# Performance work log

Hardware: AMD Instinct MI355X
Metric: run time of the kernel (lower is better)

Reference implementation:

```python
import jax, jax.numpy as jnp
import numpy as np

EPS = 1e-5
NEG_SLOPE = 0.2


def batchnorm_nodes(x, gamma, beta):
    # BatchNorm2d over channel=node axis; x: [N, T, D], stats over (T, D) per node
    m = x.mean(axis=(1, 2), keepdims=True)
    v = ((x - m) ** 2).mean(axis=(1, 2), keepdims=True)
    return (x - m) * jax.lax.rsqrt(v + EPS) * gamma[:, None, None] + beta[:, None, None]


def gat_relation(h, src, dst, W, al, ar, N):
    # h: [N, T, D]; W: [D, H, dh]; al/ar: [H, dh]
    z = jnp.einsum('ntd,dhe->nthe', h, W)              # [N, T, H, dh]
    el = jnp.einsum('nthe,he->nth', z, al)             # [N, T, H]
    er = jnp.einsum('nthe,he->nth', z, ar)
    e = jax.nn.leaky_relu(el[src] + er[dst], NEG_SLOPE)  # [E, T, H]
    emax = jax.ops.segment_max(e, dst, num_segments=N)   # [N, T, H]
    ex = jnp.exp(e - emax[dst])
    denom = jax.ops.segment_sum(ex, dst, num_segments=N)
    alpha = ex / jnp.maximum(denom[dst], 1e-16)          # segment softmax over in-edges
    msg = alpha[..., None] * z[src]                      # [E, T, H, dh]
    return jax.ops.segment_sum(msg, dst, num_segments=N)  # [N, T, H, dh]


def setup_inputs() -> dict:
    key = jax.random.key(0)
    ks = jax.random.split(key, 12)
    N, T, D, H, E, DFF = 10000, 12, 64, 4, 100000, 128
    dh = D // H
    s = 0.1
    return {
        'x': jax.random.normal(ks[0], (N, T, D), jnp.float32),
        'src1': jax.random.randint(ks[1], (E,), 0, N, jnp.int32),
        'dst1': jax.random.randint(ks[2], (E,), 0, N, jnp.int32),
        'src2': jax.random.randint(ks[3], (E,), 0, N, jnp.int32),
        'dst2': jax.random.randint(ks[4], (E,), 0, N, jnp.int32),
        'W1': jax.random.normal(ks[5], (D, H, dh), jnp.float32) * s,
        'al1': jax.random.normal(ks[6], (H, dh), jnp.float32) * s,
        'ar1': jax.random.normal(ks[7], (H, dh), jnp.float32) * s,
        'W2': jax.random.normal(ks[8], (D, H, dh), jnp.float32) * s,
        'al2': jax.random.normal(ks[9], (H, dh), jnp.float32) * s,
        'ar2': jax.random.normal(ks[10], (H, dh), jnp.float32) * s,
        'bn1_g': jnp.ones((N,), jnp.float32),
        'bn1_b': jnp.zeros((N,), jnp.float32),
        'bn2_g': jnp.ones((N,), jnp.float32),
        'bn2_b': jnp.zeros((N,), jnp.float32),
        'ff_w1': jax.random.normal(ks[11], (D, DFF), jnp.float32) * s,
        'ff_b1': jnp.zeros((DFF,), jnp.float32),
        'ff_w2': jax.random.normal(jax.random.fold_in(key, 99), (DFF, D), jnp.float32) * s,
        'ff_b2': jnp.zeros((D,), jnp.float32),
    }


def reference(x, src1, dst1, src2, dst2, W1, al1, ar1, W2, al2, ar2,
              bn1_g, bn1_b, bn2_g, bn2_b, ff_w1, ff_b1, ff_w2, ff_b2):
    N, T, D = x.shape
    h = batchnorm_nodes(x, bn1_g, bn1_b)
    # HeteroGraphConv: per-relation GAT, sum aggregation
    m = gat_relation(h, src1, dst1, W1, al1, ar1, N) \
      + gat_relation(h, src2, dst2, W2, al2, ar2, N)   # [N, T, H, dh]
    m = m.reshape(N, T, D)
    x2 = x + m                                          # residual (dropout=identity in eval)
    h2 = batchnorm_nodes(x2, bn2_g, bn2_b)
    ff = jax.nn.gelu(h2 @ ff_w1 + ff_b1, approximate=False) @ ff_w2 + ff_b2
    return x2 + ff
```

## Files before the change

### kernel.cpp

```cpp
#include <hip/hip_runtime.h>
#include <math.h>

constexpr int kT = 12;
constexpr float kNeg = 0.2f;
constexpr float kEps = 1e-5f;
constexpr float kLog2e = 1.44269504088896f;

typedef __attribute__((ext_vector_type(8))) short bf16x8;
typedef __attribute__((ext_vector_type(4))) float f32x4;

__device__ __forceinline__ short f2bf(float f) {
  union { float f; unsigned u; } v;
  v.f = f;
  return (short)((v.u + 0x7fffu + ((v.u >> 16) & 1u)) >> 16);
}
__device__ __forceinline__ unsigned pack2(float a, float b) {
  return (unsigned)(unsigned short)f2bf(a) | ((unsigned)(unsigned short)f2bf(b) << 16);
}

__device__ __forceinline__ float wave_reduce_sum(float v) {
#pragma unroll
  for (int o = 32; o > 0; o >>= 1) v += __shfl_xor(v, o);
  return v;
}

__global__ void prep_kernel(const float* __restrict__ x, const float* __restrict__ g,
                            const float* __restrict__ b, float* __restrict__ scale,
                            float* __restrict__ shift, const float* __restrict__ fw1,
                            const float* __restrict__ fw2, const float* __restrict__ zW1,
                            const float* __restrict__ zW2, const float* __restrict__ al1,
                            const float* __restrict__ ar1, const float* __restrict__ al2,
                            const float* __restrict__ ar2, bf16x8* __restrict__ fw1f,
                            bf16x8* __restrict__ fw2f, bf16x8* __restrict__ zw1f,
                            bf16x8* __restrict__ zw2f, bf16x8* __restrict__ walf,
                            const int* __restrict__ dst1, const int* __restrict__ dst2,
                            int* __restrict__ deg1, int* __restrict__ deg2, int N, int E1,
                            int E2, int nBnBlk) {
  int blk = blockIdx.x;
  int lane = threadIdx.x & 63, wid = threadIdx.x >> 6;
  if (blk < nBnBlk) {
    int n = blk * 4 + wid;
    if (n < N) {
      const float* xr = x + (size_t)n * 768;
      float s = 0.f, s2 = 0.f;
#pragma unroll
      for (int c = 0; c < 3; c++) {
        float4 v = *(const float4*)&xr[c * 256 + lane * 4];
        s += v.x + v.y + v.z + v.w;
        s2 += v.x * v.x + v.y * v.y + v.z * v.z + v.w * v.w;
      }
      s = wave_reduce_sum(s);
      s2 = wave_reduce_sum(s2);
      if (lane == 0) {
        const float inv = 1.f / 768.f;
        float mean = s * inv;
        float var = s2 * inv - mean * mean;
        float sc = rsqrtf(var + kEps) * g[n];
        scale[n] = sc;
        shift[n] = b[n] - mean * sc;
      }
    }
    return;
  }
  blk -= nBnBlk;
  int m = lane & 15, q = lane >> 4;
  if (blk == 0) {
    for (int fi = wid; fi < 16; fi += 4) {
      int mt = fi >> 1, kc = fi & 1;
      bf16x8 v;
#pragma unroll
      for (int j = 0; j < 8; j++) v[j] = f2bf(fw1[(kc * 32 + q * 8 + j) * 128 + mt * 16 + m]);
      fw1f[fi * 64 + lane] = v;
    }
    return;
  }
  if (blk == 1) {
    for (int fi = wid; fi < 16; fi += 4) {
      int mt2 = fi >> 2, kc2 = fi & 3;
      bf16x8 u;
#pragma unroll
      for (int j = 0; j < 8; j++) u[j] = f2bf(fw2[(kc2 * 32 + q * 8 + j) * 64 + mt2 * 16 + m]);
      fw2f[fi * 64 + lane] = u;
    }
    return;
  }
  if (blk == 2) {
    for (int fi = wid; fi < 8; fi += 4) {
      int mt = fi >> 1, kc = fi & 1;
      bf16x8 v, u;
#pragma unroll
      for (int j = 0; j < 8; j++) {
        int d = kc * 32 + q * 8 + j;
        v[j] = f2bf(zW1[d * 64 + mt * 16 + m]);
        u[j] = f2bf(zW2[d * 64 + mt * 16 + m]);
      }
      zw1f[fi * 64 + lane] = v;
      zw2f[fi * 64 + lane] = u;
    }
    return;
  }
  if (blk == 3) {
    __shared__ float wal[16][64];
    for (int e0 = threadIdx.x; e0 < 1024; e0 += 256) {
      int f = e0 >> 6, d = e0 & 63;
      int h = f & 3;
      const float* av = (f < 4) ? al1 : (f < 8) ? ar1 : (f < 12) ? al2 : ar2;
      const float* W = (f < 8) ? zW1 : zW2;
      float s = 0.f;
#pragma unroll
      for (int e = 0; e < 16; e++) s += W[d * 64 + h * 16 + e] * av[h * 16 + e];
      wal[f][d] = s * kLog2e;
    }
    __syncthreads();
    if (wid == 0) {
#pragma unroll
      for (int kc = 0; kc < 2; kc++) {
        bf16x8 v;
#pragma unroll
        for (int j = 0; j < 8; j++) v[j] = f2bf(wal[m][kc * 32 + q * 8 + j]);
        walf[kc * 64 + lane] = v;
      }
    }
    return;
  }
  int i = (blk - 4) * 256 + threadIdx.x;
  if (i < E1) atomicAdd(&deg1[dst1[i]], 1);
  else if (i < E1 + E2) atomicAdd(&deg2[dst2[i - E1]], 1);
}

__global__ void scan_kernel(const int* __restrict__ deg1, int* __restrict__ off1,
                            const int* __restrict__ deg2, int* __restrict__ off2, int N) {
  const int* deg = blockIdx.x ? deg2 : deg1;
  int* off = blockIdx.x ? off2 : off1;
  __shared__ int wsum[16];
  __shared__ int carry;
  int tid = threadIdx.x, lane = tid & 63, wv = tid >> 6;
  if (tid == 0) { carry = 0; off[0] = 0; }
  __syncthreads();
  for (int base = 0; base < N; base += 1024) {
    int i = base + tid;
    int incl = (i < N) ? deg[i] : 0;
#pragma unroll
    for (int o = 1; o < 64; o <<= 1) {
      int y = __shfl_up(incl, o);
      if (lane >= o) incl += y;
    }
    if (lane == 63) wsum[wv] = incl;
    __syncthreads();
    if (tid < 16) {
      int p = wsum[tid];
#pragma unroll
      for (int o = 1; o < 16; o <<= 1) {
        int y = __shfl_up(p, o);
        if (tid >= o) p += y;
      }
      wsum[tid] = p;
    }
    __syncthreads();
    int prefix = carry + (wv > 0 ? wsum[wv - 1] : 0);
    if (i < N) off[i + 1] = prefix + incl;
    int total = carry + wsum[15];
    __syncthreads();
    if (tid == 0) carry = total;
    __syncthreads();
  }
}

__global__ __launch_bounds__(256) void fillzel_kernel(
    const int* __restrict__ src1, const int* __restrict__ dst1, const int* __restrict__ off1,
    int* __restrict__ cur1, int* __restrict__ scsr1, const int* __restrict__ src2,
    const int* __restrict__ dst2, const int* __restrict__ off2, int* __restrict__ cur2,
    int* __restrict__ scsr2, int E1, int E2, int nZelBlk,
    const float* __restrict__ x, const float* __restrict__ scale,
    const float* __restrict__ shift, const bf16x8* __restrict__ zw1f,
    const bf16x8* __restrict__ zw2f, const bf16x8* __restrict__ walf,
    unsigned short* __restrict__ z1, unsigned short* __restrict__ z2,
    float* __restrict__ el1, float* __restrict__ er1, float* __restrict__ el2,
    float* __restrict__ er2, int NT) {
  if ((int)blockIdx.x >= nZelBlk) {
    int i = ((int)blockIdx.x - nZelBlk) * 256 + threadIdx.x;
    if (i < E1) {
      int d = dst1[i];
      int p = atomicAdd(&cur1[d], 1);
      scsr1[off1[d] + p] = src1[i] * kT;
    } else if (i < E1 + E2) {
      int k = i - E1;
      int d = dst2[k];
      int p = atomicAdd(&cur2[d], 1);
      scsr2[off2[d] + p] = src2[k] * kT;
    }
    return;
  }
  __shared__ bf16x8 sW1[8][64];
  __shared__ bf16x8 sW2[8][64];
  __shared__ bf16x8 sWE[2][64];
  int lane = threadIdx.x & 63, wid = threadIdx.x >> 6;
  int m = lane & 15, q = lane >> 4;
  for (int fi = wid; fi < 8; fi += 4) {
    sW1[fi][lane] = zw1f[fi * 64 + lane];
    sW2[fi][lane] = zw2f[fi * 64 + lane];
  }
  if (wid == 0) {
    sWE[0][lane] = walf[lane];
    sWE[1][lane] = walf[64 + lane];
  }
  __syncthreads();
  int ntile = (NT + 15) / 16;
  for (int tile = blockIdx.x * 4 + wid; tile < ntile; tile += nZelBlk * 4) {
    int r0 = tile * 16;
    int row = r0 + m;
    int rowc = (row < NT) ? row : NT - 1;
    int n = rowc / kT;
    float sc = scale[n], sh = shift[n];
    bf16x8 hf[2];
#pragma unroll
    for (int kc = 0; kc < 2; kc++) {
      float4 p0 = *(const float4*)&x[(size_t)rowc * 64 + kc * 32 + q * 8];
      float4 p1 = *(const float4*)&x[(size_t)rowc * 64 + kc * 32 + q * 8 + 4];
      hf[kc][0] = f2bf(fmaf(p0.x, sc, sh));
      hf[kc][1] = f2bf(fmaf(p0.y, sc, sh));
      hf[kc][2] = f2bf(fmaf(p0.z, sc, sh));
      hf[kc][3] = f2bf(fmaf(p0.w, sc, sh));
      hf[kc][4] = f2bf(fmaf(p1.x, sc, sh));
      hf[kc][5] = f2bf(fmaf(p1.y, sc, sh));
      hf[kc][6] = f2bf(fmaf(p1.z, sc, sh));
      hf[kc][7] = f2bf(fmaf(p1.w, sc, sh));
    }
    f32x4 a1[4], a2[4], ae;
#pragma unroll
    for (int mt = 0; mt < 4; mt++) {
      a1[mt] = (f32x4){0.f, 0.f, 0.f, 0.f};
      a2[mt] = (f32x4){0.f, 0.f, 0.f, 0.f};
    }
    ae = (f32x4){0.f, 0.f, 0.f, 0.f};
#pragma unroll
    for (int kc = 0; kc < 2; kc++) {
#pragma unroll
      for (int mt = 0; mt < 4; mt++) {
        a1[mt] = __builtin_amdgcn_mfma_f32_16x16x32_bf16(sW1[mt * 2 + kc][lane], hf[kc],
                                                         a1[mt], 0, 0, 0);
        a2[mt] = __builtin_amdgcn_mfma_f32_16x16x32_bf16(sW2[mt * 2 + kc][lane], hf[kc],
                                                         a2[mt], 0, 0, 0);
      }
      ae = __builtin_amdgcn_mfma_f32_16x16x32_bf16(sWE[kc][lane], hf[kc], ae, 0, 0, 0);
    }
    if (row < NT) {
      float* edst = (q == 0) ? el1 : (q == 1) ? er1 : (q == 2) ? el2 : er2;
      *(float4*)&edst[(size_t)row * 4] = make_float4(ae[0], ae[1], ae[2], ae[3]);
#pragma unroll
      for (int mt = 0; mt < 4; mt++) {
        uint2 u1 = {pack2(a1[mt][0], a1[mt][1]), pack2(a1[mt][2], a1[mt][3])};
        uint2 u2 = {pack2(a2[mt][0], a2[mt][1]), pack2(a2[mt][2], a2[mt][3])};
        *(uint2*)&z1[(size_t)row * 64 + mt * 16 + 4 * q] = u1;
        *(uint2*)&z2[(size_t)row * 64 + mt * 16 + 4 * q] = u2;
      }
    }
  }
}

__device__ __forceinline__ void gat_rel(int n, int t, const int* __restrict__ scsr,
                                        const int* __restrict__ off,
                                        const float* __restrict__ elp, float er_h,
                                        const unsigned short* __restrict__ zp, int lane,
                                        float& a0, float& a1, float& a2, float& a3) {
  int b0 = off[n], b1 = off[n + 1];
  if (b1 <= b0) return;
  float den = 0.f, n0 = 0.f, n1 = 0.f, n2 = 0.f, n3 = 0.f;
  for (int c0 = b0; c0 < b1; c0 += 64) {
    int cnt = b1 - c0;
    if (cnt > 64) cnt = 64;
    int idx = c0 + lane;
    int sbl = scsr[(idx < b1) ? idx : b1 - 1];
    int s0 = __shfl(sbl, 0) + t;
    int s1 = (cnt > 1) ? (__shfl(sbl, 1) + t) : s0;
    int s2 = (cnt > 2) ? (__shfl(sbl, 2) + t) : s1;
    float e0 = elp[(size_t)s0 * 4];
    uint2 z0 = *(const uint2*)(zp + (size_t)s0 * 64);
    float e1 = elp[(size_t)s1 * 4];
    uint2 zz1 = *(const uint2*)(zp + (size_t)s1 * 64);
    float e2 = elp[(size_t)s2 * 4];
    uint2 zz2 = *(const uint2*)(zp + (size_t)s2 * 64);
    for (int k = 0; k < cnt; k++) {
      int s3 = (k + 3 < cnt) ? (__shfl(sbl, k + 3) + t) : s2;
      float e3 = elp[(size_t)s3 * 4];
      uint2 zz3 = *(const uint2*)(zp + (size_t)s3 * 64);
      float ev = e0 + er_h;
      ev = fmaxf(ev, kNeg * ev);
      float wgt = exp2f(ev);
      den += wgt;
      n0 = fmaf(wgt, __uint_as_float(z0.x << 16), n0);
      n1 = fmaf(wgt, __uint_as_float(z0.x & 0xffff0000u), n1);
      n2 = fmaf(wgt, __uint_as_float(z0.y << 16), n2);
      n3 = fmaf(wgt, __uint_as_float(z0.y & 0xffff0000u), n3);
      s0 = s1; e0 = e1; z0 = zz1;
      s1 = s2; e1 = e2; zz1 = zz2;
      s2 = s3; e2 = e3; zz2 = zz3;
    }
  }
  float inv = 1.f / den;
  a0 = fmaf(n0, inv, a0);
  a1 = fmaf(n1, inv, a1);
  a2 = fmaf(n2, inv, a2);
  a3 = fmaf(n3, inv, a3);
}

__global__ __launch_bounds__(256) void agg_kernel(
    const float* __restrict__ x, const int* __restrict__ scsr1,
    const int* __restrict__ off1, const float* __restrict__ el1,
    const float* __restrict__ er1, const unsigned short* __restrict__ z1,
    const int* __restrict__ scsr2, const int* __restrict__ off2,
    const float* __restrict__ el2, const float* __restrict__ er2,
    const unsigned short* __restrict__ z2, float* __restrict__ x2,
    float* __restrict__ bn2s, float* __restrict__ bn2q, int N) {
  int wid = threadIdx.x >> 6, lane = threadIdx.x & 63;
  int w = blockIdx.x * 4 + wid;
  if (w >= N * 3) return;
  int n = w / 3;
  int t0 = (w - n * 3) * 4;
  int tl = lane >> 4, cg = lane & 15;
  int t = t0 + tl;
  int row = n * kT + t;
  int h = cg >> 2;
  float a0 = 0.f, a1 = 0.f, a2 = 0.f, a3 = 0.f;
  gat_rel(n, t, scsr1, off1, el1 + h, er1[(size_t)row * 4 + h], z1 + cg * 4, lane, a0, a1, a2,
          a3);
  gat_rel(n, t, scsr2, off2, el2 + h, er2[(size_t)row * 4 + h], z2 + cg * 4, lane, a0, a1, a2,
          a3);

  size_t base = (size_t)row * 64 + cg * 4;
  float4 xr = *(const float4*)&x[base];
  float4 o;
  o.x = xr.x + a0;
  o.y = xr.y + a1;
  o.z = xr.z + a2;
  o.w = xr.w + a3;
  *(float4*)&x2[base] = o;
  float s1 = o.x + o.y + o.z + o.w;
  float s2 = o.x * o.x + o.y * o.y + o.z * o.z + o.w * o.w;
  s1 = wave_reduce_sum(s1);
  s2 = wave_reduce_sum(s2);
  if (lane == 0) {
    atomicAdd(&bn2s[n], s1);
    atomicAdd(&bn2q[n], s2);
  }
}

__global__ __launch_bounds__(256, 2) void ff_kernel(
    const float* __restrict__ x2, const float* __restrict__ bn2s,
    const float* __restrict__ bn2q, const float* __restrict__ bng,
    const float* __restrict__ bnb, const bf16x8* __restrict__ w1f,
    const bf16x8* __restrict__ w2f, const float* __restrict__ b1,
    const float* __restrict__ b2, float* __restrict__ out, int NT) {
  __shared__ bf16x8 sW1[16][64];
  __shared__ bf16x8 sW2[16][64];
  __shared__ float sB1[128];
  __shared__ float sB2[64];
  int lane = threadIdx.x & 63, wid = threadIdx.x >> 6;
  int m = lane & 15, q = lane >> 4;
  {
    int fi0 = wid * 4;
#pragma unroll
    for (int k = 0; k < 4; k++) {
      sW1[fi0 + k][lane] = w1f[(fi0 + k) * 64 + lane];
      sW2[fi0 + k][lane] = w2f[(fi0 + k) * 64 + lane];
    }
    if (threadIdx.x < 128) sB1[threadIdx.x] = b1[threadIdx.x];
    if (threadIdx.x < 64) sB2[threadIdx.x] = b2[threadIdx.x];
  }
  __syncthreads();

  const float inv = 1.f / 768.f;
  int grp = blockIdx.x * 4 + wid;
  int ngrp = (NT + 31) / 32;
  if (grp >= ngrp) return;

  bf16x8 hf[2][2];
  f32x4 acc[2][8];
#pragma unroll
  for (int tt = 0; tt < 2; tt++) {
    int row = grp * 32 + tt * 16 + m;
    int rowc = (row < NT) ? row : NT - 1;
    int n = rowc / kT;
    float mean = bn2s[n] * inv;
    float var = bn2q[n] * inv - mean * mean;
    float sc = rsqrtf(var + kEps) * bng[n];
    float sh = bnb[n] - mean * sc;
#pragma unroll
    for (int kc = 0; kc < 2; kc++) {
      const float4 p0 = *(const float4*)&x2[(size_t)rowc * 64 + kc * 32 + q * 8];
      const float4 p1 = *(const float4*)&x2[(size_t)rowc * 64 + kc * 32 + q * 8 + 4];
      hf[tt][kc][0] = f2bf(fmaf(p0.x, sc, sh));
      hf[tt][kc][1] = f2bf(fmaf(p0.y, sc, sh));
      hf[tt][kc][2] = f2bf(fmaf(p0.z, sc, sh));
      hf[tt][kc][3] = f2bf(fmaf(p0.w, sc, sh));
      hf[tt][kc][4] = f2bf(fmaf(p1.x, sc, sh));
      hf[tt][kc][5] = f2bf(fmaf(p1.y, sc, sh));
      hf[tt][kc][6] = f2bf(fmaf(p1.z, sc, sh));
      hf[tt][kc][7] = f2bf(fmaf(p1.w, sc, sh));
    }
#pragma unroll
    for (int mt = 0; mt < 8; mt++) acc[tt][mt] = (f32x4){0.f, 0.f, 0.f, 0.f};
  }
#pragma unroll
  for (int kc = 0; kc < 2; kc++)
#pragma unroll
    for (int mt = 0; mt < 8; mt++)
#pragma unroll
      for (int tt = 0; tt < 2; tt++)
        acc[tt][mt] = __builtin_amdgcn_mfma_f32_16x16x32_bf16(sW1[mt * 2 + kc][lane],
                                                              hf[tt][kc], acc[tt][mt], 0, 0, 0);

  f32x4 acc2[2][4];
#pragma unroll
  for (int tt = 0; tt < 2; tt++)
#pragma unroll
    for (int mt = 0; mt < 4; mt++) acc2[tt][mt] = (f32x4){0.f, 0.f, 0.f, 0.f};
#pragma unroll
  for (int kc = 0; kc < 4; kc++) {
    float4 bb0 = *(const float4*)&sB1[(2 * kc) * 16 + 4 * q];
    float4 bb1 = *(const float4*)&sB1[(2 * kc + 1) * 16 + 4 * q];
    bf16x8 bf[2];
#pragma unroll
    for (int tt = 0; tt < 2; tt++) {
      float g0[4], g1[4];
      float u;
      u = acc[tt][2 * kc][0] + bb0.x; g0[0] = 0.5f * u * (1.f + erff(u * 0.70710678118654752f));
      u = acc[tt][2 * kc][1] + bb0.y; g0[1] = 0.5f * u * (1.f + erff(u * 0.70710678118654752f));
      u = acc[tt][2 * kc][2] + bb0.z; g0[2] = 0.5f * u * (1.f + erff(u * 0.70710678118654752f));
      u = acc[tt][2 * kc][3] + bb0.w; g0[3] = 0.5f * u * (1.f + erff(u * 0.70710678118654752f));
      u = acc[tt][2 * kc + 1][0] + bb1.x; g1[0] = 0.5f * u * (1.f + erff(u * 0.70710678118654752f));
      u = acc[tt][2 * kc + 1][1] + bb1.y; g1[1] = 0.5f * u * (1.f + erff(u * 0.70710678118654752f));
      u = acc[tt][2 * kc + 1][2] + bb1.z; g1[2] = 0.5f * u * (1.f + erff(u * 0.70710678118654752f));
      u = acc[tt][2 * kc + 1][3] + bb1.w; g1[3] = 0.5f * u * (1.f + erff(u * 0.70710678118654752f));
#pragma unroll
      for (int j = 0; j < 8; j++) {
        int srcq = (2 * q + (j >> 2)) & 3;
        int src = srcq * 16 + m;
        float v0 = __shfl(g0[j & 3], src);
        float v1 = __shfl(g1[j & 3], src);
        bf[tt][j] = f2bf((q >= 2) ? v1 : v0);
      }
    }
#pragma unroll
    for (int mt = 0; mt < 4; mt++)
#pragma unroll
      for (int tt = 0; tt < 2; tt++)
        acc2[tt][mt] = __builtin_amdgcn_mfma_f32_16x16x32_bf16(sW2[mt * 4 + kc][lane], bf[tt],
                                                               acc2[tt][mt], 0, 0, 0);
  }

#pragma unroll
  for (int tt = 0; tt < 2; tt++) {
    int row = grp * 32 + tt * 16 + m;
    if (row < NT) {
#pragma unroll
      for (int mt = 0; mt < 4; mt++) {
        size_t base = (size_t)row * 64 + mt * 16 + 4 * q;
        float4 xr = *(const float4*)&x2[base];
        float4 bb = *(const float4*)&sB2[mt * 16 + 4 * q];
        float4 o;
        o.x = acc2[tt][mt][0] + bb.x + xr.x;
        o.y = acc2[tt][mt][1] + bb.y + xr.y;
        o.z = acc2[tt][mt][2] + bb.z + xr.z;
        o.w = acc2[tt][mt][3] + bb.w + xr.w;
        *(float4*)&out[base] = o;
      }
    }
  }
}

extern "C" void kernel_launch(void* const* d_in, const int* in_sizes, int n_in,
                              void* d_out, int out_size, void* d_ws, size_t ws_size,
                              hipStream_t stream) {
  const float* x = (const float*)d_in[0];
  const int* src1 = (const int*)d_in[1];
  const int* dst1 = (const int*)d_in[2];
  const int* src2 = (const int*)d_in[3];
  const int* dst2 = (const int*)d_in[4];
  const float* W1 = (const float*)d_in[5];
  const float* al1 = (const float*)d_in[6];
  const float* ar1 = (const float*)d_in[7];
  const float* W2 = (const float*)d_in[8];
  const float* al2 = (const float*)d_in[9];
  const float* ar2 = (const float*)d_in[10];
  const float* g1 = (const float*)d_in[11];
  const float* b1 = (const float*)d_in[12];
  const float* g2 = (const float*)d_in[13];
  const float* b2 = (const float*)d_in[14];
  const float* fw1 = (const float*)d_in[15];
  const float* fb1 = (const float*)d_in[16];
  const float* fw2 = (const float*)d_in[17];
  const float* fb2 = (const float*)d_in[18];

  const int N = in_sizes[11];
  const int E1 = in_sizes[1];
  const int E2 = in_sizes[3];
  const int NT = N * kT;

  char* p = (char*)d_ws;
  auto alloc = [&](size_t bytes) -> char* {
    char* r = p;
    p += (bytes + 255) & ~(size_t)255;
    return r;
  };
  unsigned short* z1 = (unsigned short*)alloc((size_t)NT * 64 * 2);
  unsigned short* z2 = (unsigned short*)alloc((size_t)NT * 64 * 2);
  float* el1 = (float*)alloc((size_t)NT * 4 * 4);
  float* er1 = (float*)alloc((size_t)NT * 4 * 4);
  float* el2 = (float*)alloc((size_t)NT * 4 * 4);
  float* er2 = (float*)alloc((size_t)NT * 4 * 4);
  float* x2 = (float*)alloc((size_t)NT * 64 * 4);
  float* sc1 = (float*)alloc((size_t)N * 4);
  float* sh1 = (float*)alloc((size_t)N * 4);
  int* off1 = (int*)alloc((size_t)(N + 1) * 4);
  int* off2 = (int*)alloc((size_t)(N + 1) * 4);
  int* scsr1 = (int*)alloc((size_t)E1 * 4);
  int* scsr2 = (int*)alloc((size_t)E2 * 4);
  bf16x8* fw1f = (bf16x8*)alloc(16 * 64 * 16);
  bf16x8* fw2f = (bf16x8*)alloc(16 * 64 * 16);
  bf16x8* zw1f = (bf16x8*)alloc(8 * 64 * 16);
  bf16x8* zw2f = (bf16x8*)alloc(8 * 64 * 16);
  bf16x8* walf = (bf16x8*)alloc(2 * 64 * 16);
  char* zero_base = p;
  int* deg1 = (int*)alloc((size_t)N * 4);
  int* cur1 = (int*)alloc((size_t)N * 4);
  int* deg2 = (int*)alloc((size_t)N * 4);
  int* cur2 = (int*)alloc((size_t)N * 4);
  float* bn2s = (float*)alloc((size_t)N * 4);
  float* bn2q = (float*)alloc((size_t)N * 4);
  size_t zero_bytes = (size_t)(p - zero_base);
  hipMemsetAsync(zero_base, 0, zero_bytes, stream);

  const int nBnBlk = (N + 3) / 4;
  const int degBlk = (E1 + E2 + 255) / 256;
  prep_kernel<<<nBnBlk + 4 + degBlk, 256, 0, stream>>>(
      x, g1, b1, sc1, sh1, fw1, fw2, W1, W2, al1, ar1, al2, ar2, fw1f, fw2f, zw1f, zw2f, walf,
      dst1, dst2, deg1, deg2, N, E1, E2, nBnBlk);
  scan_kernel<<<2, 1024, 0, stream>>>(deg1, off1, deg2, off2, N);
  const int nZelBlk = 1875;
  fillzel_kernel<<<nZelBlk + degBlk, 256, 0, stream>>>(
      src1, dst1, off1, cur1, scsr1, src2, dst2, off2, cur2, scsr2, E1, E2, nZelBlk, x, sc1,
      sh1, zw1f, zw2f, walf, z1, z2, el1, er1, el2, er2, NT);
  agg_kernel<<<(N * 3 + 3) / 4, 256, 0, stream>>>(x, scsr1, off1, el1, er1, z1, scsr2, off2,
                                                  el2, er2, z2, x2, bn2s, bn2q, N);
  ff_kernel<<<((NT + 31) / 32 + 3) / 4, 256, 0, stream>>>(x2, bn2s, bn2q, g2, b2, fw1f, fw2f,
                                                          fb1, fb2, (float*)d_out, NT);
}
```

Measured before the change: 248.6 us.

## Process four edges per step in GAT aggregation using quad-lane DPP weight sharing

Restructures the per-edge aggregation loop so each group of four lanes computes attention weights for four different edges at once, then broadcasts them within the quad via DPP permutes. Source indices are read with scalar readlane so z loads use uniform base addresses, and accumulation uses packed float2 math. The denominator is reduced across the quad at the end. This cuts exp2 and el-load work per edge by four and aims to raise memory-level parallelism, but adds DPP traffic, masking of padded edges and more live registers.

Result: no change. 248.5 us (-0.0%).

```diff
diff --git a/kernel.cpp b/kernel.cpp
--- a/kernel.cpp
+++ b/kernel.cpp
@@ -8,6 +8,7 @@
 
 typedef __attribute__((ext_vector_type(8))) short bf16x8;
 typedef __attribute__((ext_vector_type(4))) float f32x4;
+typedef __attribute__((ext_vector_type(2))) float f32x2;
 
 __device__ __forceinline__ short f2bf(float f) {
   union { float f; unsigned u; } v;
@@ -22,6 +23,12 @@
 #pragma unroll
   for (int o = 32; o > 0; o >>= 1) v += __shfl_xor(v, o);
   return v;
+}
+
+template <int CTRL>
+__device__ __forceinline__ float qperm(float v) {
+  int i = __float_as_int(v);
+  return __int_as_float(__builtin_amdgcn_update_dpp(i, i, CTRL, 0xf, 0xf, false));
 }
 
 __global__ void prep_kernel(const float* __restrict__ x, const float* __restrict__ g,
@@ -258,50 +265,90 @@
   }
 }
 
-__device__ __forceinline__ void gat_rel(int n, int t, const int* __restrict__ scsr,
+__device__ __forceinline__ void gat_rel(int n, int t, int zvoff, const int* __restrict__ scsr,
                                         const int* __restrict__ off,
                                         const float* __restrict__ elp, float er_h,
                                         const unsigned short* __restrict__ zp, int lane,
-                                        float& a0, float& a1, float& a2, float& a3) {
+                                        int qidx, f32x2& a01, f32x2& a23) {
   int b0 = off[n], b1 = off[n + 1];
   if (b1 <= b0) return;
-  float den = 0.f, n0 = 0.f, n1 = 0.f, n2 = 0.f, n3 = 0.f;
+  float den = 0.f;
+  f32x2 n01 = {0.f, 0.f}, n23 = {0.f, 0.f};
   for (int c0 = b0; c0 < b1; c0 += 64) {
     int cnt = b1 - c0;
     if (cnt > 64) cnt = 64;
     int idx = c0 + lane;
     int sbl = scsr[(idx < b1) ? idx : b1 - 1];
-    int s0 = __shfl(sbl, 0) + t;
-    int s1 = (cnt > 1) ? (__shfl(sbl, 1) + t) : s0;
-    int s2 = (cnt > 2) ? (__shfl(sbl, 2) + t) : s1;
-    float e0 = elp[(size_t)s0 * 4];
-    uint2 z0 = *(const uint2*)(zp + (size_t)s0 * 64);
-    float e1 = elp[(size_t)s1 * 4];
-    uint2 zz1 = *(const uint2*)(zp + (size_t)s1 * 64);
-    float e2 = elp[(size_t)s2 * 4];
-    uint2 zz2 = *(const uint2*)(zp + (size_t)s2 * 64);
-    for (int k = 0; k < cnt; k++) {
-      int s3 = (k + 3 < cnt) ? (__shfl(sbl, k + 3) + t) : s2;
-      float e3 = elp[(size_t)s3 * 4];
-      uint2 zz3 = *(const uint2*)(zp + (size_t)s3 * 64);
-      float ev = e0 + er_h;
+    int sg = __shfl(sbl, qidx) + t;
+    float ecur = elp[(size_t)sg * 4];
+    uint2 zb0, zb1, zb2, zb3;
+    {
+      int s0 = __builtin_amdgcn_readlane(sbl, 0);
+      int s1 = __builtin_amdgcn_readlane(sbl, 1);
+      int s2 = __builtin_amdgcn_readlane(sbl, 2);
+      int s3 = __builtin_amdgcn_readlane(sbl, 3);
+      zb0 = *(const uint2*)(zp + (size_t)s0 * 64 + zvoff);
+      zb1 = *(const uint2*)(zp + (size_t)s1 * 64 + zvoff);
+      zb2 = *(const uint2*)(zp + (size_t)s2 * 64 + zvoff);
+      zb3 = *(const uint2*)(zp + (size_t)s3 * 64 + zvoff);
+    }
+    for (int g = 0; g < cnt; g += 4) {
+      bool more = (g + 4) < cnt;
+      float enext = 0.f;
+      uint2 zn0, zn1, zn2, zn3;
+      if (more) {
+        int sg2 = __shfl(sbl, g + 4 + qidx) + t;
+        enext = elp[(size_t)sg2 * 4];
+        int s0 = __builtin_amdgcn_readlane(sbl, g + 4);
+        int s1 = __builtin_amdgcn_readlane(sbl, g + 5);
+        int s2 = __builtin_amdgcn_readlane(sbl, g + 6);
+        int s3 = __builtin_amdgcn_readlane(sbl, g + 7);
+        zn0 = *(const uint2*)(zp + (size_t)s0 * 64 + zvoff);
+        zn1 = *(const uint2*)(zp + (size_t)s1 * 64 + zvoff);
+        zn2 = *(const uint2*)(zp + (size_t)s2 * 64 + zvoff);
+        zn3 = *(const uint2*)(zp + (size_t)s3 * 64 + zvoff);
+      }
+      float ev = ecur + er_h;
       ev = fmaxf(ev, kNeg * ev);
-      float wgt = exp2f(ev);
-      den += wgt;
-      n0 = fmaf(wgt, __uint_as_float(z0.x << 16), n0);
-      n1 = fmaf(wgt, __uint_as_float(z0.x & 0xffff0000u), n1);
-      n2 = fmaf(wgt, __uint_as_float(z0.y << 16), n2);
-      n3 = fmaf(wgt, __uint_as_float(z0.y & 0xffff0000u), n3);
-      s0 = s1; e0 = e1; z0 = zz1;
-      s1 = s2; e1 = e2; zz1 = zz2;
-      s2 = s3; e2 = e3; zz2 = zz3;
-    }
-  }
+      float w = exp2f(ev);
+      w = (g + qidx < cnt) ? w : 0.f;
+      den += w;
+      {
+        float w0 = qperm<0x00>(w);
+        float w1 = qperm<0x55>(w);
+        float w2 = qperm<0xAA>(w);
+        float w3 = qperm<0xFF>(w);
+        f32x2 v;
+        v = (f32x2){__uint_as_float(zb0.x << 16), __uint_as_float(zb0.x & 0xffff0000u)};
+        n01 += v * w0;
+        v = (f32x2){__uint_as_float(zb0.y << 16), __uint_as_float(zb0.y & 0xffff0000u)};
+        n23 += v * w0;
+        v = (f32x2){__uint_as_float(zb1.x << 16), __uint_as_float(zb1.x & 0xffff0000u)};
+        n01 += v * w1;
+        v = (f32x2){__uint_as_float(zb1.y << 16), __uint_as_float(zb1.y & 0xffff0000u)};
+        n23 += v * w1;
+        v = (f32x2){__uint_as_float(zb2.x << 16), __uint_as_float(zb2.x & 0xffff0000u)};
+        n01 += v * w2;
+        v = (f32x2){__uint_as_float(zb2.y << 16), __uint_as_float(zb2.y & 0xffff0000u)};
+        n23 += v * w2;
+        v = (f32x2){__uint_as_float(zb3.x << 16), __uint_as_float(zb3.x & 0xffff0000u)};
+        n01 += v * w3;
+        v = (f32x2){__uint_as_float(zb3.y << 16), __uint_as_float(zb3.y & 0xffff0000u)};
+        n23 += v * w3;
+      }
+      if (!more) break;
+      ecur = enext;
+      zb0 = zn0;
+      zb1 = zn1;
+      zb2 = zn2;
+      zb3 = zn3;
+    }
+  }
+  den += qperm<0xB1>(den);
+  den += qperm<0x4E>(den);
   float inv = 1.f / den;
-  a0 = fmaf(n0, inv, a0);
-  a1 = fmaf(n1, inv, a1);
-  a2 = fmaf(n2, inv, a2);
-  a3 = fmaf(n3, inv, a3);
+  a01 += n01 * inv;
+  a23 += n23 * inv;
 }
 
 __global__ __launch_bounds__(256) void agg_kernel(
@@ -321,19 +368,21 @@
   int t = t0 + tl;
   int row = n * kT + t;
   int h = cg >> 2;
-  float a0 = 0.f, a1 = 0.f, a2 = 0.f, a3 = 0.f;
-  gat_rel(n, t, scsr1, off1, el1 + h, er1[(size_t)row * 4 + h], z1 + cg * 4, lane, a0, a1, a2,
-          a3);
-  gat_rel(n, t, scsr2, off2, el2 + h, er2[(size_t)row * 4 + h], z2 + cg * 4, lane, a0, a1, a2,
-          a3);
+  int qidx = lane & 3;
+  int zvoff = t * 64 + cg * 4;
+  f32x2 a01 = {0.f, 0.f}, a23 = {0.f, 0.f};
+  gat_rel(n, t, zvoff, scsr1, off1, el1 + h, er1[(size_t)row * 4 + h], z1, lane, qidx, a01,
+          a23);
+  gat_rel(n, t, zvoff, scsr2, off2, el2 + h, er2[(size_t)row * 4 + h], z2, lane, qidx, a01,
+          a23);
 
   size_t base = (size_t)row * 64 + cg * 4;
   float4 xr = *(const float4*)&x[base];
   float4 o;
-  o.x = xr.x + a0;
-  o.y = xr.y + a1;
-  o.z = xr.z + a2;
-  o.w = xr.w + a3;
+  o.x = xr.x + a01.x;
+  o.y = xr.y + a01.y;
+  o.z = xr.z + a23.x;
+  o.w = xr.w + a23.y;
   *(float4*)&x2[base] = o;
   float s1 = o.x + o.y + o.z + o.w;
   float s2 = o.x * o.x + o.y * o.y + o.z * o.z + o.w * o.w;
```
